# Kernel tuning notes

Hardware: AMD Instinct MI355X
Metric: run time of the kernel (lower is better)

## Reference

```python
import jax, jax.numpy as jnp
import numpy as np

N = 100000   # nodes
E = 1200000  # edges
C = 64       # in_channels
H = 64       # hidden_channels
OUT = 10     # out_channels
G = 128      # graphs in batch
L = 3        # num_conv_layers
EPS = 1e-5   # BatchNorm eps


def batchnorm(x, g, b):
    # training-mode BatchNorm1d: biased batch stats over the node/graph axis
    mu = x.mean(axis=0)
    var = x.var(axis=0)
    return (x - mu) * jax.lax.rsqrt(var + EPS) * g + b


def _gcn_norm(edge_index):
    # add self-loops (weight 1) then symmetric normalization deg^-1/2 * w * deg^-1/2
    loop = jnp.arange(N)
    src = jnp.concatenate([edge_index[0], loop])
    dst = jnp.concatenate([edge_index[1], loop])
    w = jnp.ones((E + N,), jnp.float32)
    deg = jax.ops.segment_sum(w, src, num_segments=N)
    dis = jnp.where(deg > 0, jax.lax.rsqrt(deg), 0.0)
    norm = dis[src] * w * dis[dst]
    return src, dst, norm


def gcn_conv(h, W, b, src, dst, norm):
    # linear transform -> gather source features -> edge-normalize -> scatter-add to dst
    hw = h @ W
    msg = norm[:, None] * hw[src]          # [E+N, H]
    return jax.ops.segment_sum(msg, dst, num_segments=N) + b


def setup_inputs() -> dict:
    key = jax.random.key(0)
    ks = jax.random.split(key, 8)
    s = 0.1
    return {
        'x': jax.random.normal(ks[0], (N, C), jnp.float32),
        'edge_index': jax.random.randint(ks[1], (2, E), 0, N),
        'batch_idx': jnp.sort(jax.random.randint(ks[2], (N,), 0, G)),
        # BN params initialized as in the module: weight=1, bias=1e-4
        'bn_feat_g': jnp.ones((C,), jnp.float32),
        'bn_feat_b': jnp.full((C,), 1e-4, jnp.float32),
        'W_feat': jax.random.normal(ks[3], (C, H), jnp.float32) * s,  # conv_feat (gfn=True -> pure linear)
        'b_feat': jnp.zeros((H,), jnp.float32),
        'conv_bn_g': jnp.ones((L, H), jnp.float32),
        'conv_bn_b': jnp.full((L, H), 1e-4, jnp.float32),
        'conv_W': jax.random.normal(ks[4], (L, H, H), jnp.float32) * s,
        'conv_b': jnp.zeros((L, H), jnp.float32),
        'bn_fc_g': jnp.ones((H,), jnp.float32),
        'bn_fc_b': jnp.full((H,), 1e-4, jnp.float32),
        'W_fc': jax.random.normal(ks[5], (H, H), jnp.float32) * s,
        'b_fc': jnp.zeros((H,), jnp.float32),
        'bn_hid_g': jnp.ones((H,), jnp.float32),
        'bn_hid_b': jnp.full((H,), 1e-4, jnp.float32),
        'W_cls': jax.random.normal(ks[6], (H, OUT), jnp.float32) * s,
        'b_cls': jnp.zeros((OUT,), jnp.float32),
    }


def reference(x, edge_index, batch_idx, bn_feat_g, bn_feat_b, W_feat, b_feat,
              conv_bn_g, conv_bn_b, conv_W, conv_b, bn_fc_g, bn_fc_b, W_fc, b_fc,
              bn_hid_g, bn_hid_b, W_cls, b_cls):
    src, dst, norm = _gcn_norm(edge_index)
    # forward_BNConvReLU, residual=False, gating=None, xg=None, dropout=0
    h = batchnorm(x, bn_feat_g, bn_feat_b)
    h = jax.nn.relu(h @ W_feat + b_feat)           # conv_feat: gfn=True => linear only
    for i in range(L):
        h_ = batchnorm(h, conv_bn_g[i], conv_bn_b[i])
        h = jax.nn.relu(gcn_conv(h_, conv_W[i], conv_b[i], src, dst, norm))
    hg = jax.ops.segment_sum(h, batch_idx, num_segments=G)  # global_add_pool -> [G, H]
    h_ = batchnorm(hg, bn_fc_g, bn_fc_b)
    hg = jax.nn.relu(h_ @ W_fc + b_fc)
    hg = batchnorm(hg, bn_hid_g, bn_hid_b)
    logits = hg @ W_cls + b_cls
    return jax.nn.log_softmax(logits, axis=-1)
```

## Files before the change

kernel.cpp:

```cpp
#include <hip/hip_runtime.h>
#include <hip/hip_fp16.h>

#define N_NODES 100000
#define N_EDGES 1200000
#define GRAPHS 128
#define EPSBN 1e-5f


__global__ __launch_bounds__(256) void k_build(const int* __restrict__ src,
                                               const int* __restrict__ dst,
                                               int* __restrict__ cnt,
                                               int* __restrict__ deg,
                                               int* __restrict__ ecsr) {
    int e = blockIdx.x * 256 + threadIdx.x;
    if (e < N_EDGES) {
        int s = src[e], d = dst[e];
        atomicAdd(&deg[s], 1);
        int p = atomicAdd(&cnt[d], 1);
        ecsr[(d << 6) + p] = s;
    }
}

__global__ __launch_bounds__(256) void k_dis(const int* __restrict__ deg,
                                             float* __restrict__ dis) {
    int i = blockIdx.x * 256 + threadIdx.x;
    if (i < N_NODES) dis[i] = rsqrtf((float)deg[i] + 1.0f);
}


__global__ __launch_bounds__(256) void k_sigma(const float* __restrict__ dis,
                                               const int* __restrict__ cnt,
                                               const int* __restrict__ ecsr,
                                               float* __restrict__ sigma) {
    int lane = threadIdx.x & 63;
    int wid = threadIdx.x >> 6;
    for (int node = blockIdx.x * 4 + wid; node < N_NODES; node += gridDim.x * 4) {
        int m = cnt[node];
        int sraw = ecsr[(node << 6) + lane];
        float dd = dis[node];
        int sL = (lane < m) ? sraw : 0;
        float v = (lane < m) ? dis[sL] : 0.f;
#pragma unroll
        for (int d = 1; d <= 32; d <<= 1) v += __shfl_xor(v, d, 64);
        if (lane == 0) sigma[node] = dd * (v + dd);
    }
}


__global__ __launch_bounds__(256) void k_stats(const float* __restrict__ x,
                                               float* __restrict__ sums) {
    const float4* x4 = (const float4*)x;
    int t = threadIdx.x;
    int q = t & 15, rg = t >> 4;
    float4 s = {0.f, 0.f, 0.f, 0.f}, s2 = {0.f, 0.f, 0.f, 0.f};
    for (int r = blockIdx.x * 16 + rg; r < N_NODES; r += gridDim.x * 16) {
        float4 v = x4[r * 16 + q];
        s.x += v.x; s.y += v.y; s.z += v.z; s.w += v.w;
        s2.x += v.x * v.x; s2.y += v.y * v.y; s2.z += v.z * v.z; s2.w += v.w * v.w;
    }
    __shared__ float red[2][16][64];
    red[0][rg][q * 4 + 0] = s.x;  red[0][rg][q * 4 + 1] = s.y;
    red[0][rg][q * 4 + 2] = s.z;  red[0][rg][q * 4 + 3] = s.w;
    red[1][rg][q * 4 + 0] = s2.x; red[1][rg][q * 4 + 1] = s2.y;
    red[1][rg][q * 4 + 2] = s2.z; red[1][rg][q * 4 + 3] = s2.w;
    __syncthreads();
    if (t < 64) {
        float a = 0.f, b = 0.f;
#pragma unroll
        for (int k = 0; k < 16; k++) { a += red[0][k][t]; b += red[1][k][t]; }
        atomicAdd(&sums[t], a);
        atomicAdd(&sums[64 + t], b);
    }
}


__global__ __launch_bounds__(256) void k_fold(const float* __restrict__ sums, const float* __restrict__ g,
                       const float* __restrict__ b, const float* __restrict__ W,
                       const float* __restrict__ bias_in, int has_bias,
                       float* __restrict__ Wout, float* __restrict__ bout) {
    __shared__ float a[64], cc[64];
    int t = threadIdx.x;
    if (t < 64) {
        float mu = sums[t] * (1.0f / N_NODES);
        float var = sums[64 + t] * (1.0f / N_NODES) - mu * mu;
        float av = g[t] * rsqrtf(var + EPSBN);
        a[t] = av;
        cc[t] = b[t] - mu * av;
    }
    __syncthreads();
    for (int i = t; i < 4096; i += 256) Wout[i] = a[i >> 6] * W[i];
    if (t < 64) {
        float acc = has_bias ? bias_in[t] : 0.0f;
        for (int k = 0; k < 64; k++) acc += cc[k] * W[k * 64 + t];
        bout[t] = acc;
    }
}


__global__ __launch_bounds__(256, 4) void k_gemm2(const float* __restrict__ X, const float* __restrict__ W,
                        const float* __restrict__ bias, const float* __restrict__ dis,
                        __half* __restrict__ U,
                        float* __restrict__ sums, int do_stats) {
    int t = threadIdx.x;
    int j = t & 63;
    int rg = t >> 6;
    __shared__ float wlds[64][64];
    __shared__ float xs[16][64];
    for (int i = t; i < 4096; i += 256) wlds[i >> 6][i & 63] = W[i];
    float bj = bias[j];
    __syncthreads();
    float s_sum = 0.f, s_sq = 0.f;
    for (int base = blockIdx.x * 16; base < N_NODES; base += gridDim.x * 16) {
        ((float4*)xs)[t] = ((const float4*)(X + base * 64))[t];
        int r0 = rg * 4;
        float a0 = bj, a1 = bj, a2 = bj, a3 = bj;
        const float4* x0 = (const float4*)xs[r0 + 0];
        const float4* x1 = (const float4*)xs[r0 + 1];
        const float4* x2 = (const float4*)xs[r0 + 2];
        const float4* x3 = (const float4*)xs[r0 + 3];
#pragma unroll
        for (int q4 = 0; q4 < 16; q4++) {
            float w0 = wlds[q4 * 4 + 0][j], w1 = wlds[q4 * 4 + 1][j];
            float w2 = wlds[q4 * 4 + 2][j], w3 = wlds[q4 * 4 + 3][j];
            float4 v0 = x0[q4]; a0 += v0.x * w0 + v0.y * w1 + v0.z * w2 + v0.w * w3;
            float4 v1 = x1[q4]; a1 += v1.x * w0 + v1.y * w1 + v1.z * w2 + v1.w * w3;
            float4 v2 = x2[q4]; a2 += v2.x * w0 + v2.y * w1 + v2.z * w2 + v2.w * w3;
            float4 v3 = x3[q4]; a3 += v3.x * w0 + v3.y * w1 + v3.z * w2 + v3.w * w3;
        }
        a0 = fmaxf(a0, 0.f); a1 = fmaxf(a1, 0.f);
        a2 = fmaxf(a2, 0.f); a3 = fmaxf(a3, 0.f);
        int nb = base + r0;
        U[(nb + 0) * 64 + j] = __float2half_rn(a0 * dis[nb + 0]);
        U[(nb + 1) * 64 + j] = __float2half_rn(a1 * dis[nb + 1]);
        U[(nb + 2) * 64 + j] = __float2half_rn(a2 * dis[nb + 2]);
        U[(nb + 3) * 64 + j] = __float2half_rn(a3 * dis[nb + 3]);
        if (do_stats) {
            s_sum += a0 + a1 + a2 + a3;
            s_sq += a0 * a0 + a1 * a1 + a2 * a2 + a3 * a3;
        }
    }
    if (do_stats) {
        __syncthreads();
        xs[rg][j] = s_sum;
        xs[4 + rg][j] = s_sq;
        __syncthreads();
        if (t < 64) {
            atomicAdd(&sums[t], xs[0][t] + xs[1][t] + xs[2][t] + xs[3][t]);
            atomicAdd(&sums[64 + t], xs[4][t] + xs[5][t] + xs[6][t] + xs[7][t]);
        }
    }
}


__global__ __launch_bounds__(256, 4) void k_aggemm(const __half* __restrict__ u,
                        const float* __restrict__ dis, const float* __restrict__ sigma,
                        const int* __restrict__ cnt, const int* __restrict__ ecsr,
                        const float* __restrict__ sums_in, const float* __restrict__ bng,
                        const float* __restrict__ bnb,
                        const float* __restrict__ W, const float* __restrict__ bias,
                        __half* __restrict__ uout, float* __restrict__ hout, int last,
                        float* __restrict__ sums_out, int do_stats) {
    const __half2* u2 = (const __half2*)u;
    int t = threadIdx.x;
    int j = t & 63;
    int wid = t >> 6;
    int g = j >> 5, c = j & 31;
    __shared__ float wlds[64][64];
    __shared__ float xs[16][64];
    if (t < 64) {
        float mu = sums_in[t] * (1.0f / N_NODES);
        float var = sums_in[64 + t] * (1.0f / N_NODES) - mu * mu;
        float av = bng[t] * rsqrtf(var + EPSBN);
        xs[0][t] = av;
        xs[1][t] = bnb[t] - mu * av;
    }
    __syncthreads();
    for (int i = t; i < 4096; i += 256) wlds[i >> 6][i & 63] = W[i] * xs[0][i >> 6];
    float cb = 0.f;
#pragma unroll 8
    for (int q = 0; q < 64; q++) cb += xs[1][q] * W[q * 64 + j];
    float bj = bias[j];
    __syncthreads();
    float s_sum = 0.f, s_sq = 0.f;
    for (int base = blockIdx.x * 16; base < N_NODES; base += gridDim.x * 16) {
        int r0 = wid * 4;
        int nb = base + r0;
        int mm[4], srw[4];
        float dvals[4], svals[4];
        __half2 selfs[4];
#pragma unroll
        for (int r = 0; r < 4; r++) {
            mm[r] = cnt[nb + r];
            srw[r] = ecsr[((nb + r) << 6) + j];
            dvals[r] = dis[nb + r];
            svals[r] = sigma[nb + r];
            selfs[r] = u2[(nb + r) * 32 + c];
        }
#pragma unroll
        for (int r = 0; r < 4; r++) {
            int m = mm[r];
            int sL = (j < m) ? srw[r] : 0;
            float ax = 0.f, ay = 0.f;
#pragma unroll
            for (int k = 0; k < 8; k++) {
                int e = 2 * k + g;
                int sE = __shfl(sL, e, 64);
                float w = (e < m) ? 1.0f : 0.0f;
                float2 f = __half22float2(u2[sE * 32 + c]);
                ax += w * f.x; ay += w * f.y;
            }
            if (m > 16) {
                for (int e = 16 + g; e < m; e += 2) {
                    int sE = __shfl(sL, e, 64);
                    float2 f = __half22float2(u2[sE * 32 + c]);
                    ax += f.x; ay += f.y;
                }
            }
            ax += __shfl_xor(ax, 32, 64);
            ay += __shfl_xor(ay, 32, 64);
            if (g == 0) {
                float2 sf = __half22float2(selfs[r]);
                float dd = dvals[r];
                xs[r0 + r][2 * c + 0] = dd * (ax + sf.x);
                xs[r0 + r][2 * c + 1] = dd * (ay + sf.y);
            }
        }
        float a0 = bj + svals[0] * cb, a1 = bj + svals[1] * cb;
        float a2 = bj + svals[2] * cb, a3 = bj + svals[3] * cb;
        const float4* x0 = (const float4*)xs[r0 + 0];
        const float4* x1 = (const float4*)xs[r0 + 1];
        const float4* x2 = (const float4*)xs[r0 + 2];
        const float4* x3 = (const float4*)xs[r0 + 3];
#pragma unroll
        for (int q4 = 0; q4 < 16; q4++) {
            float w0 = wlds[q4 * 4 + 0][j], w1 = wlds[q4 * 4 + 1][j];
            float w2 = wlds[q4 * 4 + 2][j], w3 = wlds[q4 * 4 + 3][j];
            float4 v0 = x0[q4]; a0 += v0.x * w0 + v0.y * w1 + v0.z * w2 + v0.w * w3;
            float4 v1 = x1[q4]; a1 += v1.x * w0 + v1.y * w1 + v1.z * w2 + v1.w * w3;
            float4 v2 = x2[q4]; a2 += v2.x * w0 + v2.y * w1 + v2.z * w2 + v2.w * w3;
            float4 v3 = x3[q4]; a3 += v3.x * w0 + v3.y * w1 + v3.z * w2 + v3.w * w3;
        }
        a0 = fmaxf(a0, 0.f); a1 = fmaxf(a1, 0.f);
        a2 = fmaxf(a2, 0.f); a3 = fmaxf(a3, 0.f);
        if (last) {
            hout[(nb + 0) * 64 + j] = a0;
            hout[(nb + 1) * 64 + j] = a1;
            hout[(nb + 2) * 64 + j] = a2;
            hout[(nb + 3) * 64 + j] = a3;
        } else {
            uout[(nb + 0) * 64 + j] = __float2half_rn(a0 * dvals[0]);
            uout[(nb + 1) * 64 + j] = __float2half_rn(a1 * dvals[1]);
            uout[(nb + 2) * 64 + j] = __float2half_rn(a2 * dvals[2]);
            uout[(nb + 3) * 64 + j] = __float2half_rn(a3 * dvals[3]);
        }
        if (do_stats) {
            s_sum += a0 + a1 + a2 + a3;
            s_sq += a0 * a0 + a1 * a1 + a2 * a2 + a3 * a3;
        }
    }
    if (do_stats) {
        __syncthreads();
        xs[wid][j] = s_sum;
        xs[4 + wid][j] = s_sq;
        __syncthreads();
        if (t < 64) {
            atomicAdd(&sums_out[t], xs[0][t] + xs[1][t] + xs[2][t] + xs[3][t]);
            atomicAdd(&sums_out[64 + t], xs[4][t] + xs[5][t] + xs[6][t] + xs[7][t]);
        }
    }
}


__global__ __launch_bounds__(256) void k_pool(const float* __restrict__ h, const int* __restrict__ batch,
                       float* __restrict__ hg) {
    int g = blockIdx.x >> 2, q3 = blockIdx.x & 3;
    int lo = 0, hi = N_NODES;
    while (lo < hi) { int m = (lo + hi) >> 1; if (batch[m] < g) lo = m + 1; else hi = m; }
    int start = lo;
    lo = start; hi = N_NODES;
    while (lo < hi) { int m = (lo + hi) >> 1; if (batch[m] < g + 1) lo = m + 1; else hi = m; }
    int end = lo;
    int len = end - start;
    int c0 = start + ((len * q3) >> 2);
    int c1 = start + ((len * (q3 + 1)) >> 2);
    int c = threadIdx.x & 63, rg = threadIdx.x >> 6;
    float s = 0.f;
    for (int r = c0 + rg; r < c1; r += 4) s += h[r * 64 + c];
    __shared__ float ls[4][64];
    ls[rg][c] = s;
    __syncthreads();
    if (rg == 0) atomicAdd(&hg[g * 64 + c], ls[0][c] + ls[1][c] + ls[2][c] + ls[3][c]);
}


__global__ __launch_bounds__(512) void k_tail(const float* __restrict__ hg_in,
                       const float* __restrict__ g1, const float* __restrict__ b1,
                       const float* __restrict__ Wfc, const float* __restrict__ bfc,
                       const float* __restrict__ g2, const float* __restrict__ b2,
                       const float* __restrict__ Wcls, const float* __restrict__ bcls,
                       float* __restrict__ out) {
    __shared__ float hgn[8192];
    __shared__ float h2[8192];
    __shared__ float red[2][8][64];
    __shared__ float a[64], cc[64];
    __shared__ float Wc[640];
    __shared__ float logits[1280];
    __shared__ float lse[128];
    int t = threadIdx.x;
    int j = t & 63;
    int w = t >> 6;

    {
        float su = 0.f, sq = 0.f;
#pragma unroll
        for (int gg = 0; gg < 16; gg++) {
            float v = hg_in[(w * 16 + gg) * 64 + j];
            su += v; sq += v * v;
        }
        red[0][w][j] = su; red[1][w][j] = sq;
    }
    for (int i = t; i < 640; i += 512) Wc[i] = Wcls[i];
    __syncthreads();
    if (t < 64) {
        float su = 0.f, sq = 0.f;
#pragma unroll
        for (int k = 0; k < 8; k++) { su += red[0][k][t]; sq += red[1][k][t]; }
        float mu = su * (1.f / 128.f);
        float var = sq * (1.f / 128.f) - mu * mu;
        float av = g1[t] * rsqrtf(var + EPSBN);
        a[t] = av; cc[t] = b1[t] - mu * av;
    }
    __syncthreads();
    for (int i = t; i < 8192; i += 512) hgn[i] = hg_in[i] * a[i & 63] + cc[i & 63];

    float wreg[64];
#pragma unroll
    for (int q = 0; q < 64; q++) wreg[q] = Wfc[q * 64 + j];
    float bj = bfc[j];
    __syncthreads();

    float acc[16];
#pragma unroll
    for (int r = 0; r < 16; r++) acc[r] = bj;
    const float4* hgn4 = (const float4*)hgn;
#pragma unroll
    for (int q4 = 0; q4 < 16; q4++) {
#pragma unroll
        for (int r = 0; r < 16; r++) {
            float4 hv = hgn4[(w * 16 + r) * 16 + q4];
            acc[r] += hv.x * wreg[q4 * 4 + 0] + hv.y * wreg[q4 * 4 + 1]
                    + hv.z * wreg[q4 * 4 + 2] + hv.w * wreg[q4 * 4 + 3];
        }
    }
    float s = 0.f, s2 = 0.f;
#pragma unroll
    for (int r = 0; r < 16; r++) {
        float v = fmaxf(acc[r], 0.f);
        h2[(w * 16 + r) * 64 + j] = v;
        s += v; s2 += v * v;
    }
    red[0][w][j] = s; red[1][w][j] = s2;
    __syncthreads();

    if (t < 64) {
        float su = 0.f, sq = 0.f;
#pragma unroll
        for (int k = 0; k < 8; k++) { su += red[0][k][t]; sq += red[1][k][t]; }
        float mu = su * (1.f / 128.f);
        float var = sq * (1.f / 128.f) - mu * mu;
        float av = g2[t] * rsqrtf(var + EPSBN);
        a[t] = av; cc[t] = b2[t] - mu * av;
    }
    __syncthreads();
    for (int i = t; i < 8192; i += 512) h2[i] = h2[i] * a[i & 63] + cc[i & 63];
    __syncthreads();

    for (int idx = t; idx < 1280; idx += 512) {
        int row = idx / 10, o = idx - row * 10;
        float v = bcls[o];
#pragma unroll
        for (int q = 0; q < 64; q++) v += h2[row * 64 + q] * Wc[q * 10 + o];
        logits[idx] = v;
    }
    __syncthreads();
    if (t < 128) {
        float mx = -1e30f;
#pragma unroll
        for (int o = 0; o < 10; o++) mx = fmaxf(mx, logits[t * 10 + o]);
        float se = 0.f;
#pragma unroll
        for (int o = 0; o < 10; o++) se += expf(logits[t * 10 + o] - mx);
        lse[t] = mx + logf(se);
    }
    __syncthreads();
    for (int idx = t; idx < 1280; idx += 512) out[idx] = logits[idx] - lse[idx / 10];
}


extern "C" void kernel_launch(void* const* d_in, const int* in_sizes, int n_in,
                              void* d_out, int out_size, void* d_ws, size_t ws_size,
                              hipStream_t stream) {
    const float* x         = (const float*)d_in[0];
    const int*   ei        = (const int*)  d_in[1];
    const int*   batch     = (const int*)  d_in[2];
    const float* bn_feat_g = (const float*)d_in[3];
    const float* bn_feat_b = (const float*)d_in[4];
    const float* W_feat    = (const float*)d_in[5];
    const float* b_feat    = (const float*)d_in[6];
    const float* conv_bn_g = (const float*)d_in[7];
    const float* conv_bn_b = (const float*)d_in[8];
    const float* conv_W    = (const float*)d_in[9];
    const float* conv_b    = (const float*)d_in[10];
    const float* bn_fc_g   = (const float*)d_in[11];
    const float* bn_fc_b   = (const float*)d_in[12];
    const float* W_fc      = (const float*)d_in[13];
    const float* b_fc      = (const float*)d_in[14];
    const float* bn_hid_g  = (const float*)d_in[15];
    const float* bn_hid_b  = (const float*)d_in[16];
    const float* W_cls     = (const float*)d_in[17];
    const float* b_cls     = (const float*)d_in[18];
    float* out = (float*)d_out;

    float* ws    = (float*)d_ws;
    float* hbuf  = ws;
    __half* u_a  = (__half*)(ws + 6400000);
    __half* u_b  = (__half*)(ws + 9600000);
    float* dis   = ws + 12800000;
    float* sigma = ws + 12900000;
    float* Wt    = ws + 13000000;
    float* bt    = Wt + 4096;
    float* hg    = bt + 64;
    float* sums  = hg + 8192;
    int*   cnt   = (int*)(sums + 640);
    int*   ecsr  = cnt + 100000;
    int*   deg   = (int*)u_b;

    float* sx = sums;
    float* s0 = sums + 128;
    float* s1 = sums + 256;
    float* s2 = sums + 384;

    const int* srcp = ei;
    const int* dstp = ei + N_EDGES;

    hipMemsetAsync(hg, 0, (8192 + 640 + 100000) * sizeof(float), stream);
    hipMemsetAsync(deg, 0, 100000 * sizeof(int), stream);

    k_build<<<(N_EDGES + 255) / 256, 256, 0, stream>>>(srcp, dstp, cnt, deg, ecsr);
    k_dis<<<(N_NODES + 255) / 256, 256, 0, stream>>>(deg, dis);
    k_sigma<<<1024, 256, 0, stream>>>(dis, cnt, ecsr, sigma);

    k_stats<<<512, 256, 0, stream>>>(x, sx);
    k_fold<<<1, 256, 0, stream>>>(sx, bn_feat_g, bn_feat_b, W_feat, b_feat, 1, Wt, bt);
    k_gemm2<<<2048, 256, 0, stream>>>(x, Wt, bt, dis, u_a, s0, 1);

    k_aggemm<<<2048, 256, 0, stream>>>(u_a, dis, sigma, cnt, ecsr,
                                       s0, conv_bn_g + 0, conv_bn_b + 0,
                                       conv_W + 0, conv_b + 0,
                                       u_b, nullptr, 0, s1, 1);
    k_aggemm<<<2048, 256, 0, stream>>>(u_b, dis, sigma, cnt, ecsr,
                                       s1, conv_bn_g + 64, conv_bn_b + 64,
                                       conv_W + 4096, conv_b + 64,
                                       u_a, nullptr, 0, s2, 1);
    k_aggemm<<<2048, 256, 0, stream>>>(u_a, dis, sigma, cnt, ecsr,
                                       s2, conv_bn_g + 128, conv_bn_b + 128,
                                       conv_W + 8192, conv_b + 128,
                                       nullptr, hbuf, 1, nullptr, 0);

    k_pool<<<4 * GRAPHS, 256, 0, stream>>>(hbuf, batch, hg);
    k_tail<<<1, 512, 0, stream>>>(hg, bn_fc_g, bn_fc_b, W_fc, b_fc,
                                  bn_hid_g, bn_hid_b, W_cls, b_cls, out);
}
```

Before: 552.4 us.

## Partition edges into destination shards before CSR scatter to localize atomics

```diff
diff --git a/kernel.cpp b/kernel.cpp
--- a/kernel.cpp
+++ b/kernel.cpp
@@ -5,19 +5,63 @@
 #define N_EDGES 1200000
 #define GRAPHS 128
 #define EPSBN 1e-5f
-
-
-__global__ __launch_bounds__(256) void k_build(const int* __restrict__ src,
-                                               const int* __restrict__ dst,
-                                               int* __restrict__ cnt,
-                                               int* __restrict__ deg,
-                                               int* __restrict__ ecsr) {
-    int e = blockIdx.x * 256 + threadIdx.x;
-    if (e < N_EDGES) {
+#define NSHARD 8
+#define SH_NODES 12500
+#define NSUB 8
+#define CAP_SUB 24576
+
+
+__global__ __launch_bounds__(256) void k_part(const int* __restrict__ src,
+                                              const int* __restrict__ dst,
+                                              int* __restrict__ deg,
+                                              int* __restrict__ cur,
+                                              long long* __restrict__ ebuf) {
+    int t = threadIdx.x;
+    int lane = t & 63;
+    int gw = (blockIdx.x * 4 + (t >> 6)) & (NSUB - 1);
+    for (int e = blockIdx.x * 256 + t; e < N_EDGES; e += gridDim.x * 256) {
         int s = src[e], d = dst[e];
         atomicAdd(&deg[s], 1);
-        int p = atomicAdd(&cnt[d], 1);
-        ecsr[(d << 6) + p] = s;
+        int b = d / SH_NODES;
+        long long pack = ((long long)d << 32) | (unsigned)s;
+#pragma unroll
+        for (int bb = 0; bb < NSHARD; bb++) {
+            unsigned long long mask = __ballot(b == bb);
+            if (mask) {
+                int cnt = __popcll(mask);
+                int leader = __ffsll((long long)mask) - 1;
+                int base = 0;
+                if (lane == leader) base = atomicAdd(&cur[bb * NSUB + gw], cnt);
+                base = __shfl(base, leader, 64);
+                if (b == bb) {
+                    int off = __popcll(mask & ((1ULL << lane) - 1));
+                    if (base + off < CAP_SUB)
+                        ebuf[(bb * NSUB + gw) * CAP_SUB + base + off] = pack;
+                }
+            }
+        }
+    }
+}
+
+
+__global__ __launch_bounds__(256) void k_scat(const long long* __restrict__ ebuf,
+                                              const int* __restrict__ cur,
+                                              int* __restrict__ cnt,
+                                              int* __restrict__ ecsr) {
+    int shard = blockIdx.x & (NSHARD - 1);
+    int bpos = blockIdx.x >> 3;
+    int t = threadIdx.x;
+    for (int sub = 0; sub < NSUB; sub++) {
+        int n = cur[shard * NSUB + sub];
+        if (n > CAP_SUB) n = CAP_SUB;
+        const long long* base = ebuf + (shard * NSUB + sub) * CAP_SUB;
+        for (int i = bpos * 256 + t; i < n; i += 64 * 256) {
+            long long pack = base[i];
+            int d = (int)(pack >> 32);
+            int s = (int)(pack & 0xffffffffLL);
+            int p = atomicAdd(&cnt[d], 1);
+            ecsr[(d << 6) + p] = s;
+        }
     }
 }
 
@@ -97,7 +141,7 @@
 }
 
 
-__global__ __launch_bounds__(256, 4) void k_gemm2(const float* __restrict__ X, const float* __restrict__ W,
+__global__ __launch_bounds__(256, 5) void k_gemm2(const float* __restrict__ X, const float* __restrict__ W,
                         const float* __restrict__ bias, const float* __restrict__ dis,
                         __half* __restrict__ U,
                         float* __restrict__ sums, int do_stats) {
@@ -152,7 +196,7 @@
 }
 
 
-__global__ __launch_bounds__(256, 4) void k_aggemm(const __half* __restrict__ u,
+__global__ __launch_bounds__(256, 5) void k_aggemm(const __half* __restrict__ u,
                         const float* __restrict__ dis, const float* __restrict__ sigma,
                         const int* __restrict__ cnt, const int* __restrict__ ecsr,
                         const float* __restrict__ sums_in, const float* __restrict__ bng,
@@ -434,6 +478,8 @@
     int*   cnt   = (int*)(sums + 640);
     int*   ecsr  = cnt + 100000;
     int*   deg   = (int*)u_b;
+    long long* ebuf = (long long*)hbuf;
+    int*   cur   = (int*)(sums + 512);
 
     float* sx = sums;
     float* s0 = sums + 128;
@@ -446,7 +492,8 @@
     hipMemsetAsync(hg, 0, (8192 + 640 + 100000) * sizeof(float), stream);
     hipMemsetAsync(deg, 0, 100000 * sizeof(int), stream);
 
-    k_build<<<(N_EDGES + 255) / 256, 256, 0, stream>>>(srcp, dstp, cnt, deg, ecsr);
+    k_part<<<2048, 256, 0, stream>>>(srcp, dstp, deg, cur, ebuf);
+    k_scat<<<512, 256, 0, stream>>>(ebuf, cur, cnt, ecsr);
     k_dis<<<(N_NODES + 255) / 256, 256, 0, stream>>>(deg, dis);
     k_sigma<<<1024, 256, 0, stream>>>(dis, cnt, ecsr, sigma);
 
```

Result: slower. 1.446 ms (+161.7%).
